# Performance work log

Measured on AMD Instinct MI355X. Metric: run time of the kernel, lower is better.

## Reference

```python
import jax, jax.numpy as jnp
import numpy as np

WD, WH, WW = 2, 7, 7          # window size (d, h, w)
N = WD * WH * WW              # 98 tokens per window
DIM = 768
NH = 24
HD = DIM // NH                # 32
SCALE = HD ** -0.5
NW = 64                       # windows per image
B = 4
B_ = B * NW                   # 256


def _relative_position_index():
    d, h, w = np.meshgrid(np.arange(WD), np.arange(WH), np.arange(WW), indexing='ij')
    coords = np.stack([d.ravel(), h.ravel(), w.ravel()])        # (3, N)
    rel = (coords[:, :, None] - coords[:, None, :]).transpose(1, 2, 0)  # (N, N, 3)
    rel = rel + np.array([WD - 1, WH - 1, WW - 1])
    rel = rel * np.array([(2 * WH - 1) * (2 * WW - 1), 2 * WW - 1, 1])
    return rel.sum(-1).astype(np.int32)                         # (N, N)


def setup_inputs() -> dict:
    key = jax.random.key(0)
    ks = jax.random.split(key, 5)
    table_rows = (2 * WD - 1) * (2 * WH - 1) * (2 * WW - 1)     # 507
    return {
        'x': jax.random.normal(ks[0], (B_, N, DIM), jnp.float32),
        'mask': jax.random.normal(ks[1], (NW, N, N), jnp.float32),
        'qkv_w': jax.random.normal(ks[2], (3 * DIM, DIM), jnp.float32) * 0.02,
        'qkv_b': jax.random.normal(ks[3], (3 * DIM,), jnp.float32) * 0.02,
        'rel_table': jax.random.normal(ks[4], (table_rows, NH), jnp.float32) * 0.02,
        'rel_index': jnp.asarray(_relative_position_index()),
    }


def reference(x, mask, qkv_w, qkv_b, rel_table, rel_index):
    Bs, n, c = x.shape
    # qkv linear; einops '(nH hD qkv)' => last dim factored as (nH, hD, 3)
    qkv = x @ qkv_w.T + qkv_b                                   # (Bs, N, 3C)
    qkv = qkv.reshape(Bs, n, NH, HD, 3)
    q, k, v = (jnp.moveaxis(qkv, -1, 0)                         # (3, Bs, N, nH, hD)
                  .transpose(0, 1, 3, 2, 4))                    # (3, Bs, nH, N, hD)
    attn = jnp.einsum('bhqd,bhkd->bhqk', q, k) * SCALE          # (Bs, nH, N, N)
    bias = rel_table[rel_index]                                 # (N, N, nH)
    attn = attn + bias.transpose(2, 0, 1)[None]                 # + (1, nH, N, N)
    # window mask add
    attn = attn.reshape(Bs // NW, NW, NH, n, n) + mask[None, :, None]
    attn = attn.reshape(Bs, NH, n, n)
    attn = jax.nn.softmax(attn, axis=-1)
    out = jnp.einsum('bhqk,bhkd->bhqd', attn, v)                # (Bs, nH, N, hD)
    return out.transpose(0, 2, 1, 3).reshape(Bs, n, c)          # (Bs, N, C)
```

## Files before the change

kernel.cpp:

```cpp
#include <hip/hip_runtime.h>
#include <hip/hip_bf16.h>
#include <stdint.h>


#define NTOK 98
#define MT 7
#define NPAD 112
#define DIMX 768
#define NHEAD 24
#define HDIM 32
#define NQKV 2304
#define BROWS 25088
#define SCALE 0.17677669529663689f
#define LOG2E 1.4426950408889634f
#define SCL2E (SCALE * LOG2E)
#define NN2 (NTOK * NTOK)
#define BMROW 112
#define BMSZ (BMROW * BMROW)
#define BMQ (BMSZ / 4)
#define PLANE ((size_t)BROWS * HDIM)

#define NB_X 18816
#define NB_W 1728
#define NB_BA 294
#define NB_B2 2352
#define GEMM_BLKS 3528

#if __has_builtin(__builtin_amdgcn_exp2f)
#define EXP2F(x) __builtin_amdgcn_exp2f(x)
#else
#define EXP2F(x) exp2f(x)
#endif

typedef __attribute__((ext_vector_type(8))) short short8;
typedef __attribute__((ext_vector_type(4))) short short4v;
typedef __attribute__((ext_vector_type(4))) float floatx4;

__device__ __forceinline__ short f2b(float f) {
    __hip_bfloat16 h = __float2bfloat16(f);
    return __builtin_bit_cast(short, h);
}
__device__ __forceinline__ float b2f(unsigned short s) {
    return __builtin_bit_cast(float, ((unsigned)s) << 16);
}

__device__ __forceinline__ void gload_lds16(const void* g, void* l) {
    __builtin_amdgcn_global_load_lds(
        (const __attribute__((address_space(1))) void*)g,
        (__attribute__((address_space(3))) void*)l, 16, 0, 0);
}

__device__ __forceinline__ void bm_body(int t,
                                        const float* __restrict__ rel_table,
                                        const int* __restrict__ rel_index,
                                        const float* __restrict__ mask,
                                        short* __restrict__ bm) {
    int wh = t / BMQ;
    int r4 = t % BMQ;
    int i = r4 / 28;
    int j0 = (r4 % 28) * 4;
    int h = wh % NHEAD, w = wh / NHEAD;
    short4v o;
    #pragma unroll
    for (int jj = 0; jj < 4; ++jj) {
        int j = j0 + jj;
        float val = -1e30f;
        if (i < NTOK && j < NTOK) {
            float bv = rel_table[(size_t)rel_index[i * NTOK + j] * NHEAD + h];
            float mv = mask[(size_t)w * NN2 + i * NTOK + j];
            val = (bv + mv) * LOG2E;
        }
        o[jj] = f2b(val);
    }
    *(short4v*)(bm + (size_t)wh * BMSZ + i * BMROW + j0) = o;
}

__global__ void prep_kernel(const float* __restrict__ x,
                            const float* __restrict__ w,
                            const float* __restrict__ rel_table,
                            const int* __restrict__ rel_index,
                            short* __restrict__ xb,
                            short* __restrict__ wb,
                            float* __restrict__ biasA) {
    int bid = blockIdx.x;
    if (bid < NB_X) {
        int i = bid * 256 + threadIdx.x;
        float4 f = ((const float4*)x)[i];
        short4v s = { f2b(f.x), f2b(f.y), f2b(f.z), f2b(f.w) };
        ((short4v*)xb)[i] = s;
    } else if (bid < NB_X + NB_W) {
        int i = (bid - NB_X) * 256 + threadIdx.x;
        int cp = i / 192, k4 = i % 192;
        int s = cp / DIMX, rem = cp % DIMX;
        int orig = (rem >> 5) * 96 + (rem & 31) * 3 + s;
        float sc = (s == 0) ? SCL2E : 1.0f;
        float4 f = ((const float4*)(w + (size_t)orig * DIMX))[k4];
        short4v o = { f2b(f.x * sc), f2b(f.y * sc), f2b(f.z * sc), f2b(f.w * sc) };
        ((short4v*)(wb + (size_t)cp * DIMX))[k4] = o;
    } else {
        int t = (bid - NB_X - NB_W) * 256 + threadIdx.x;
        int h = t / BMQ;
        int r4 = t % BMQ;
        int i = r4 / 28, j0 = (r4 % 28) * 4;
        float4 o;
        #pragma unroll
        for (int jj = 0; jj < 4; ++jj) {
            int j = j0 + jj;
            float val = -1e30f;
            if (i < NTOK && j < NTOK)
                val = rel_table[(size_t)rel_index[i * NTOK + j] * NHEAD + h] * LOG2E;
            o[jj] = val;
        }
        ((float4*)biasA)[t] = o;
    }
}

__global__ void bm_kernel(const float* __restrict__ rel_table,
                          const int* __restrict__ rel_index,
                          const float* __restrict__ mask,
                          short* __restrict__ bm) {
    int t = blockIdx.x * 256 + threadIdx.x;
    if (t >= 64 * NHEAD * BMQ) return;
    bm_body(t, rel_table, rel_index, mask, bm);
}

__global__ void bias_gather_kernel(const float* __restrict__ rel_table,
                                   const int* __restrict__ rel_index,
                                   float* __restrict__ bias_pre) {
    int t = blockIdx.x * 256 + threadIdx.x;
    if (t >= NHEAD * NN2) return;
    int h  = t / NN2;
    int ij = t % NN2;
    bias_pre[t] = rel_table[(size_t)rel_index[ij] * NHEAD + h];
}

__global__ void gemm_kernel(const short* __restrict__ xb,
                            const short* __restrict__ wb,
                            const float* __restrict__ qkv_b,
                            short* __restrict__ qkv,
                            const float* __restrict__ biasA,
                            const float* __restrict__ mask,
                            short* __restrict__ bm) {
    if (blockIdx.x >= GEMM_BLKS) {
        int base = (blockIdx.x - GEMM_BLKS) * 256 + threadIdx.x;
        #pragma unroll
        for (int it = 0; it < 8; ++it) {
            int t = base + it * (NB_B2 * 256);
            int wh = t / BMQ;
            int r4 = t % BMQ;
            int i = r4 / 28, j0 = (r4 % 28) * 4;
            int h = wh % NHEAD, w = wh / NHEAD;
            float4 ba = ((const float4*)biasA)[h * BMQ + r4];
            float m0 = 0.f, m1 = 0.f, m2 = 0.f, m3 = 0.f;
            if (i < NTOK && j0 < NTOK) {
                const float* mrow = mask + (size_t)w * NN2 + i * NTOK + j0;
                float2 a = *(const float2*)mrow;
                m0 = a.x; m1 = a.y;
                if (j0 < 96) {
                    float2 c = *(const float2*)(mrow + 2);
                    m2 = c.x; m3 = c.y;
                }
            }
            short4v o = { f2b(ba.x + m0 * LOG2E), f2b(ba.y + m1 * LOG2E),
                          f2b(ba.z + m2 * LOG2E), f2b(ba.w + m3 * LOG2E) };
            ((short4v*)bm)[t] = o;
        }
        return;
    }
    __shared__ short At[128 * 64];
    __shared__ short Bt[128 * 64];
    const int tid  = threadIdx.x;
    const int lane = tid & 63;
    const int wv   = tid >> 6;
    const int wr   = wv >> 1, wc = wv & 1;
    const int l15  = lane & 15;
    const int l4   = lane >> 4;

    int bid = blockIdx.x;
    int swz = (bid & 7) * 441 + (bid >> 3);
    const int mtile = swz / 18;
    const int ntile = swz % 18;

    const short* aB = xb + (size_t)(mtile * 128) * DIMX;
    const short* bB = wb + (size_t)(ntile * 128) * DIMX;
    const int lrow = lane >> 3;
    const int lcs  = (((lane & 7) ^ lrow) * 8);
    const int sa   = (l15 & 7) << 3;

    floatx4 acc[4][4];
    #pragma unroll
    for (int m = 0; m < 4; ++m)
        #pragma unroll
        for (int n = 0; n < 4; ++n) acc[m][n] = (floatx4){0.f, 0.f, 0.f, 0.f};

    for (int kb = 0; kb < 12; ++kb) {
        #pragma unroll
        for (int j = 0; j < 4; ++j) {
            int r = wv * 32 + j * 8;
            gload_lds16(aB + (size_t)(r + lrow) * DIMX + kb * 64 + lcs, &At[r * 64]);
            gload_lds16(bB + (size_t)(r + lrow) * DIMX + kb * 64 + lcs, &Bt[r * 64]);
        }
        __syncthreads();
        #pragma unroll
        for (int kh = 0; kh < 2; ++kh) {
            int k0 = kh * 32 + l4 * 8;
            int k0s = k0 ^ sa;
            short8 af[4], bfr[4];
            #pragma unroll
            for (int m = 0; m < 4; ++m)
                af[m] = *(const short8*)(&At[(wr * 64 + m * 16 + l15) * 64 + k0s]);
            #pragma unroll
            for (int n = 0; n < 4; ++n)
                bfr[n] = *(const short8*)(&Bt[(wc * 64 + n * 16 + l15) * 64 + k0s]);
            #pragma unroll
            for (int m = 0; m < 4; ++m)
                #pragma unroll
                for (int n = 0; n < 4; ++n)
                    acc[m][n] = __builtin_amdgcn_mfma_f32_16x16x32_bf16(
                        af[m], bfr[n], acc[m][n], 0, 0, 0);
        }
        __syncthreads();
    }

    #pragma unroll
    for (int n = 0; n < 4; ++n) {
        int col = ntile * 128 + wc * 64 + n * 16 + l15;
        int s = col / DIMX, rem = col % DIMX;
        int h2 = rem >> 5, d = rem & 31;
        int orig = h2 * 96 + d * 3 + s;
        float bias = qkv_b[orig] * ((s == 0) ? SCL2E : 1.0f);
        short* base = qkv + (size_t)(s * NHEAD + h2) * PLANE + d;
        #pragma unroll
        for (int m = 0; m < 4; ++m) {
            int row0 = mtile * 128 + wr * 64 + m * 16 + l4 * 4;
            #pragma unroll
            for (int r = 0; r < 4; ++r)
                base[(size_t)(row0 + r) * HDIM] = f2b(acc[m][n][r] + bias);
        }
    }
}

struct __align__(16) SMemC {
    short P[NPAD * 128];
    short q[NPAD * HDIM];
    short k[NPAD * HDIM];
    short vt[HDIM * 128];
};

__global__ __launch_bounds__(256, 3) void attn_kernel5(
    const short* __restrict__ qkv,
    const short* __restrict__ bm,
    float* __restrict__ out) {
    __shared__ SMemC sm;
    const int tid  = threadIdx.x;
    const int lane = tid & 63;
    const int wv   = tid >> 6;
    const int l15  = lane & 15;
    const int l4   = lane >> 4;
    int id = blockIdx.x;
    int nb = (id & 7) * 768 + (id >> 3);
    const int b = nb / NHEAD;
    const int h = nb % NHEAD;
    const short* qh = qkv + (size_t)h * PLANE            + (size_t)b * NTOK * HDIM;
    const short* kh = qkv + (size_t)(NHEAD + h) * PLANE  + (size_t)b * NTOK * HDIM;
    const short* vh = qkv + (size_t)(2 * NHEAD + h) * PLANE + (size_t)b * NTOK * HDIM;

    #pragma unroll
    for (int it = 0; it < 2; ++it) {
        int row0 = it * 64 + wv * 16;
        if (row0 < NTOK) {
            if (lane < (NTOK - row0) * 4) {
                gload_lds16(qh + row0 * HDIM + lane * 8, &sm.q[row0 * HDIM]);
                gload_lds16(kh + row0 * HDIM + lane * 8, &sm.k[row0 * HDIM]);
            }
        }
    }
    if (tid < 196) {
        int t = (tid >> 2) * 2, dh = tid & 3;
        const short* vp = vh + t * HDIM + dh * 8;
        short8 va = *(const short8*)vp;
        short8 vb = *(const short8*)(vp + HDIM);
        #pragma unroll
        for (int j = 0; j < 8; ++j) {
            int d = dh * 8 + j;
            int csw = t ^ ((d & 7) << 3);
            unsigned pk = ((unsigned)(unsigned short)vb[j] << 16) |
                          (unsigned)(unsigned short)va[j];
            *(unsigned*)(&sm.vt[d * 128 + csw]) = pk;
        }
    }
    if (tid < 112) {
        int a = tid / 56, r2 = (tid % 56) >> 2, seg = (tid & 3) * 8;
        short* dst = (a ? sm.k : sm.q) + (NTOK + r2) * HDIM + seg;
        *(uint4*)dst = (uint4){0u, 0u, 0u, 0u};
    }
    for (int t = tid; t < HDIM * 30; t += 256) {
        int d = t / 30, c = NTOK + t % 30;
        sm.vt[d * 128 + (c ^ ((d & 7) << 3))] = 0;
    }
    for (int t = tid; t < NPAD * 16; t += 256) {
        int r = t >> 4, c = 112 + (t & 15);
        sm.P[r * 128 + (c ^ ((r & 7) << 3))] = 0;
    }
    __syncthreads();

    int mt[2];
    mt[0] = wv;
    mt[1] = (wv + 4 < MT) ? (wv + 4) : wv;

    floatx4 sacc[2][7];
    #pragma unroll
    for (int i = 0; i < 2; ++i)
        #pragma unroll
        for (int j = 0; j < 7; ++j) sacc[i][j] = (floatx4){0.f, 0.f, 0.f, 0.f};
    {
        int k0 = l4 * 8;
        short8 bq[2];
        #pragma unroll
        for (int iq = 0; iq < 2; ++iq)
            bq[iq] = *(const short8*)(&sm.q[(mt[iq] * 16 + l15) * HDIM + k0]);
        __builtin_amdgcn_s_setprio(1);
        #pragma unroll
        for (int kt = 0; kt < 7; ++kt) {
            short8 ak = *(const short8*)(&sm.k[(kt * 16 + l15) * HDIM + k0]);
            #pragma unroll
            for (int iq = 0; iq < 2; ++iq)
                sacc[iq][kt] = __builtin_amdgcn_mfma_f32_16x16x32_bf16(
                    ak, bq[iq], sacc[iq][kt], 0, 0, 0);
        }
        __builtin_amdgcn_s_setprio(0);
    }

    const short* bmh = bm + ((size_t)(b & 63) * NHEAD + h) * BMSZ;
    const int swzp = (l15 & 7) << 3;

    #pragma unroll
    for (int iq = 0; iq < 2; ++iq) {
        int q = mt[iq] * 16 + l15;
        const short* bmq = bmh + q * BMROW + l4 * 4;
        float vv[7][4];
        #pragma unroll
        for (int kt = 0; kt < 7; ++kt) {
            short4v bm4 = *(const short4v*)(bmq + kt * 16);
            #pragma unroll
            for (int r = 0; r < 4; ++r)
                vv[kt][r] = sacc[iq][kt][r] + b2f((unsigned short)bm4[r]);
        }
        float mx = vv[0][0];
        #pragma unroll
        for (int kt = 0; kt < 7; ++kt)
            #pragma unroll
            for (int r = 0; r < 4; ++r) mx = fmaxf(mx, vv[kt][r]);
        mx = fmaxf(mx, __shfl_xor(mx, 16));
        mx = fmaxf(mx, __shfl_xor(mx, 32));
        float s = 0.f;
        #pragma unroll
        for (int kt = 0; kt < 7; ++kt)
            #pragma unroll
            for (int r = 0; r < 4; ++r) {
                float e = EXP2F(vv[kt][r] - mx);
                vv[kt][r] = e;
                s += e;
            }
        s += __shfl_xor(s, 16);
        s += __shfl_xor(s, 32);
        float inv = (q < NTOK) ? 1.f / s : 0.f;
        #pragma unroll
        for (int kt = 0; kt < 7; ++kt) {
            short4v pw = { f2b(vv[kt][0] * inv), f2b(vv[kt][1] * inv),
                           f2b(vv[kt][2] * inv), f2b(vv[kt][3] * inv) };
            *(short4v*)(&sm.P[q * 128 + ((kt * 16 + l4 * 4) ^ swzp)]) = pw;
        }
    }
    __syncthreads();

    floatx4 oacc[2][2];
    #pragma unroll
    for (int i = 0; i < 2; ++i)
        #pragma unroll
        for (int j = 0; j < 2; ++j) oacc[i][j] = (floatx4){0.f, 0.f, 0.f, 0.f};

    __builtin_amdgcn_s_setprio(1);
    #pragma unroll
    for (int kt = 0; kt < 4; ++kt) {
        int kk = (kt * 32 + l4 * 8) ^ swzp;
        short8 ap[2];
        #pragma unroll
        for (int im = 0; im < 2; ++im)
            ap[im] = *(const short8*)(&sm.P[(mt[im] * 16 + l15) * 128 + kk]);
        #pragma unroll
        for (int nt = 0; nt < 2; ++nt) {
            short8 bv = *(const short8*)(&sm.vt[(nt * 16 + l15) * 128 + kk]);
            #pragma unroll
            for (int im = 0; im < 2; ++im)
                oacc[im][nt] = __builtin_amdgcn_mfma_f32_16x16x32_bf16(
                    ap[im], bv, oacc[im][nt], 0, 0, 0);
        }
    }
    __builtin_amdgcn_s_setprio(0);

    float* ob = out + (size_t)b * NTOK * DIMX + h * HDIM;
    #pragma unroll
    for (int im = 0; im < 2; ++im)
        #pragma unroll
        for (int nt = 0; nt < 2; ++nt) {
            int dd = nt * 16 + l15;
            #pragma unroll
            for (int r = 0; r < 4; ++r) {
                int tok = mt[im] * 16 + l4 * 4 + r;
                if (tok < NTOK)
                    ob[(size_t)tok * DIMX + dd] = oacc[im][nt][r];
            }
        }
}

struct __align__(16) SMemF {
    union {
        struct {
            short xt[NPAD * 64];
            short wt[96 * 64];
        } p1;
        short P[NPAD * 128];
    } u;
    short q[NPAD * HDIM];
    short k[NPAD * HDIM];
    short vt[HDIM * 128];
};

__global__ __launch_bounds__(256, 3) void attn_fused(
    const float* __restrict__ x,
    const float* __restrict__ mask,
    const float* __restrict__ qkv_w,
    const float* __restrict__ qkv_b,
    const float* __restrict__ bias_pre,
    const float* __restrict__ rel_table,
    const int* __restrict__ rel_index,
    float* __restrict__ out) {
    __shared__ SMemF sm;
    const int tid  = threadIdx.x;
    const int lane = tid & 63;
    const int wv   = tid >> 6;
    const int l15  = lane & 15;
    const int l4   = lane >> 4;
    const int b = blockIdx.x / NHEAD;
    const int h = blockIdx.x % NHEAD;
    const float* xp = x + (size_t)b * NTOK * DIMX;
    const float* wp = qkv_w + (size_t)h * 96 * DIMX;
    int mt[2];
    mt[0] = wv;
    mt[1] = (wv + 4 < MT) ? (wv + 4) : wv;

    floatx4 acc[2][6];
    #pragma unroll
    for (int i = 0; i < 2; ++i)
        #pragma unroll
        for (int j = 0; j < 6; ++j) acc[i][j] = (floatx4){0.f, 0.f, 0.f, 0.f};

    for (int kb = 0; kb < 12; ++kb) {
        for (int t = tid; t < NTOK * 16; t += 256) {
            int row = t >> 4, c = t & 15;
            float4 f = *(const float4*)(xp + (size_t)row * DIMX + kb * 64 + c * 4);
            short4v s = { f2b(f.x), f2b(f.y), f2b(f.z), f2b(f.w) };
            *(short4v*)(&sm.u.p1.xt[row * 64 + c * 4]) = s;
        }
        for (int t = tid; t < 96 * 16; t += 256) {
            int row = t >> 4, c = t & 15;
            float4 f = *(const float4*)(wp + (size_t)row * DIMX + kb * 64 + c * 4);
            short4v s = { f2b(f.x), f2b(f.y), f2b(f.z), f2b(f.w) };
            *(short4v*)(&sm.u.p1.wt[row * 64 + c * 4]) = s;
        }
        if (tid < 14 * 8) {
            int row = 98 + (tid >> 3), c = tid & 7;
            uint4 z = {0u, 0u, 0u, 0u};
            *(uint4*)(&sm.u.p1.xt[row * 64 + c * 8]) = z;
        }
        __syncthreads();
        #pragma unroll
        for (int ks = 0; ks < 2; ++ks) {
            int k0 = ks * 32 + l4 * 8;
            short8 aM[2];
            #pragma unroll
            for (int im = 0; im < 2; ++im)
                aM[im] = *(const short8*)(&sm.u.p1.xt[(mt[im] * 16 + l15) * 64 + k0]);
            #pragma unroll
            for (int nt = 0; nt < 6; ++nt) {
                short8 bN = *(const short8*)(&sm.u.p1.wt[(nt * 16 + l15) * 64 + k0]);
                #pragma unroll
                for (int im = 0; im < 2; ++im)
                    acc[im][nt] = __builtin_amdgcn_mfma_f32_16x16x32_bf16(
                        aM[im], bN, acc[im][nt], 0, 0, 0);
            }
        }
        __syncthreads();
    }

    #pragma unroll
    for (int im = 0; im < 2; ++im)
        #pragma unroll
        for (int nt = 0; nt < 6; ++nt) {
            int col = nt * 16 + l15;
            int d = col / 3, s = col % 3;
            float bias = qkv_b[h * 96 + col];
            #pragma unroll
            for (int r = 0; r < 4; ++r) {
                int tok = mt[im] * 16 + l4 * 4 + r;
                short val = f2b(acc[im][nt][r] + bias);
                if (s == 0)      sm.q[tok * HDIM + d] = val;
                else if (s == 1) sm.k[tok * HDIM + d] = val;
                else             sm.vt[d * 128 + tok] = val;
            }
        }
    __syncthreads();
    for (int t = tid; t < HDIM * 30; t += 256) {
        int d = t / 30, c = 98 + t % 30;
        sm.vt[d * 128 + c] = 0;
    }
    for (int t = tid; t < NPAD * 16; t += 256) {
        int row = t >> 4, c = 112 + (t & 15);
        sm.u.P[row * 128 + c] = 0;
    }

    floatx4 sacc[2][7];
    #pragma unroll
    for (int i = 0; i < 2; ++i)
        #pragma unroll
        for (int j = 0; j < 7; ++j) sacc[i][j] = (floatx4){0.f, 0.f, 0.f, 0.f};
    {
        int k0 = l4 * 8;
        short8 aq[2];
        #pragma unroll
        for (int im = 0; im < 2; ++im)
            aq[im] = *(const short8*)(&sm.q[(mt[im] * 16 + l15) * HDIM + k0]);
        #pragma unroll
        for (int nt = 0; nt < 7; ++nt) {
            short8 bk = *(const short8*)(&sm.k[(nt * 16 + l15) * HDIM + k0]);
            #pragma unroll
            for (int im = 0; im < 2; ++im)
                sacc[im][nt] = __builtin_amdgcn_mfma_f32_16x16x32_bf16(
                    aq[im], bk, sacc[im][nt], 0, 0, 0);
        }
    }

    const float* biash = bias_pre ? (bias_pre + (size_t)h * NN2) : nullptr;
    const size_t moff = (size_t)(b & 63) * NN2;

    #pragma unroll
    for (int im = 0; im < 2; ++im)
        #pragma unroll
        for (int r = 0; r < 4; ++r) {
            int row = mt[im] * 16 + l4 * 4 + r;
            bool vrow = row < NTOK;
            float v[7];
            #pragma unroll
            for (int nt = 0; nt < 7; ++nt) {
                int j = nt * 16 + l15;
                bool vj = vrow && (j < NTOK);
                float bmv = 0.f;
                if (vj) {
                    float bias = biash ? biash[row * NTOK + j]
                        : rel_table[(size_t)rel_index[row * NTOK + j] * NHEAD + h];
                    bmv = bias + mask[moff + row * NTOK + j];
                }
                v[nt] = vj ? sacc[im][nt][r] * SCALE + bmv : -1e30f;
            }
            float mx = v[0];
            #pragma unroll
            for (int nt = 1; nt < 7; ++nt) mx = fmaxf(mx, v[nt]);
            #pragma unroll
            for (int off = 1; off < 16; off <<= 1) mx = fmaxf(mx, __shfl_xor(mx, off));
            float s = 0.f;
            #pragma unroll
            for (int nt = 0; nt < 7; ++nt) {
                float e = (v[nt] > -1e29f) ? __expf(v[nt] - mx) : 0.f;
                v[nt] = e;
                s += e;
            }
            #pragma unroll
            for (int off = 1; off < 16; off <<= 1) s += __shfl_xor(s, off);
            float inv = vrow ? 1.f / s : 0.f;
            #pragma unroll
            for (int nt = 0; nt < 7; ++nt)
                sm.u.P[row * 128 + nt * 16 + l15] = f2b(v[nt] * inv);
        }
    __syncthreads();

    floatx4 oacc[2][2];
    #pragma unroll
    for (int i = 0; i < 2; ++i)
        #pragma unroll
        for (int j = 0; j < 2; ++j) oacc[i][j] = (floatx4){0.f, 0.f, 0.f, 0.f};
    #pragma unroll
    for (int kt = 0; kt < 4; ++kt) {
        int kk = kt * 32 + l4 * 8;
        short8 ap[2];
        #pragma unroll
        for (int im = 0; im < 2; ++im)
            ap[im] = *(const short8*)(&sm.u.P[(mt[im] * 16 + l15) * 128 + kk]);
        #pragma unroll
        for (int nt = 0; nt < 2; ++nt) {
            short8 bv = *(const short8*)(&sm.vt[(nt * 16 + l15) * 128 + kk]);
            #pragma unroll
            for (int im = 0; im < 2; ++im)
                oacc[im][nt] = __builtin_amdgcn_mfma_f32_16x16x32_bf16(
                    ap[im], bv, oacc[im][nt], 0, 0, 0);
        }
    }
    float* ob = out + (size_t)b * NTOK * DIMX + h * HDIM;
    #pragma unroll
    for (int im = 0; im < 2; ++im)
        #pragma unroll
        for (int nt = 0; nt < 2; ++nt) {
            int dd = nt * 16 + l15;
            #pragma unroll
            for (int r = 0; r < 4; ++r) {
                int tok = mt[im] * 16 + l4 * 4 + r;
                if (tok < NTOK)
                    ob[(size_t)tok * DIMX + dd] = oacc[im][nt][r];
            }
        }
}

extern "C" void kernel_launch(void* const* d_in, const int* in_sizes, int n_in,
                              void* d_out, int out_size, void* d_ws, size_t ws_size,
                              hipStream_t stream) {
    const float* x = (const float*)d_in[0];
    const float* mask = (const float*)d_in[1];
    const float* qkv_w = (const float*)d_in[2];
    const float* qkv_b = (const float*)d_in[3];
    const float* rel_table = (const float*)d_in[4];
    const int* rel_index = (const int*)d_in[5];
    for (int i = 0; i < n_in; ++i) {
        switch (in_sizes[i]) {
            case 256 * NTOK * DIMX:  x         = (const float*)d_in[i]; break;
            case 64 * NN2:           mask      = (const float*)d_in[i]; break;
            case 3 * DIMX * DIMX:    qkv_w     = (const float*)d_in[i]; break;
            case 3 * DIMX:           qkv_b     = (const float*)d_in[i]; break;
            case 507 * NHEAD:        rel_table = (const float*)d_in[i]; break;
            case NN2:                rel_index = (const int*)d_in[i]; break;
            default: break;
        }
    }
    float* out = (float*)d_out;

    const size_t xb_bytes    = (size_t)BROWS * DIMX * 2;
    const size_t wb_bytes    = (size_t)NQKV * DIMX * 2;
    const size_t qkv_bytes   = (size_t)BROWS * NQKV * 2;
    const size_t bm_bytes    = (size_t)64 * NHEAD * BMSZ * 2;
    const size_t biasA_bytes = (size_t)NHEAD * BMSZ * 4;
    const size_t total       = xb_bytes + wb_bytes + qkv_bytes;

    if (ws_size >= total + bm_bytes + biasA_bytes) {
        short* xb    = (short*)d_ws;
        short* wb    = (short*)((char*)d_ws + xb_bytes);
        short* qkv   = (short*)((char*)d_ws + xb_bytes + wb_bytes);
        short* bmp   = (short*)((char*)d_ws + total);
        float* biasA = (float*)((char*)d_ws + total + bm_bytes);

        prep_kernel<<<NB_X + NB_W + NB_BA, 256, 0, stream>>>(
            x, qkv_w, rel_table, rel_index, xb, wb, biasA);
        gemm_kernel<<<GEMM_BLKS + NB_B2, 256, 0, stream>>>(
            xb, wb, qkv_b, qkv, biasA, mask, bmp);
        attn_kernel5<<<256 * NHEAD, 256, 0, stream>>>(qkv, bmp, out);
    } else if (ws_size >= total) {
        short* xb  = (short*)d_ws;
        short* wb  = (short*)((char*)d_ws + xb_bytes);
        short* qkv = (short*)((char*)d_ws + xb_bytes + wb_bytes);
        short* bmp = (short*)d_ws;

        prep_kernel<<<NB_X + NB_W, 256, 0, stream>>>(
            x, qkv_w, rel_table, rel_index, xb, wb, nullptr);
        gemm_kernel<<<GEMM_BLKS, 256, 0, stream>>>(
            xb, wb, qkv_b, qkv, nullptr, mask, nullptr);
        int nbm = 64 * NHEAD * BMQ;
        bm_kernel<<<(nbm + 255) / 256, 256, 0, stream>>>(
            rel_table, rel_index, mask, bmp);
        attn_kernel5<<<256 * NHEAD, 256, 0, stream>>>(qkv, bmp, out);
    } else {
        const size_t bias_bytes = (size_t)NHEAD * NN2 * sizeof(float);
        float* bias_pre = (ws_size >= bias_bytes) ? (float*)d_ws : nullptr;
        if (bias_pre) {
            int nb = NHEAD * NN2;
            bias_gather_kernel<<<(nb + 255) / 256, 256, 0, stream>>>(rel_table, rel_index, bias_pre);
        }
        attn_fused<<<256 * NHEAD, 256, 0, stream>>>(x, mask, qkv_w, qkv_b,
                                                    bias_pre, rel_table, rel_index, out);
    }
}
```

Measured before the change: 310.2 us.

## Fuse mask add into attention kernel and drop precomputed bias-mask tensor

The per-window, per-head bf16 bias+mask tensor that the GEMM kernel used to build is removed. The attention kernel now reads the fp32 per-head relative bias and the raw fp32 mask directly and adds them in registers. The block-to-window mapping is also changed so that blocks on the same XCD share windows and heads, which should let mask and bias reads hit in L2. This removes a large write and read of the intermediate, in exchange for more global loads per attention block and bounds-checked mask loads. In the fallback path, biasA now aliases the start of the workspace, which also holds xb.

```diff
diff --git a/kernel.cpp b/kernel.cpp
--- a/kernel.cpp
+++ b/kernel.cpp
@@ -23,7 +23,6 @@
 #define NB_X 18816
 #define NB_W 1728
 #define NB_BA 294
-#define NB_B2 2352
 #define GEMM_BLKS 3528
 
 #if __has_builtin(__builtin_amdgcn_exp2f)
@@ -40,9 +39,6 @@
     __hip_bfloat16 h = __float2bfloat16(f);
     return __builtin_bit_cast(short, h);
 }
-__device__ __forceinline__ float b2f(unsigned short s) {
-    return __builtin_bit_cast(float, ((unsigned)s) << 16);
-}
 
 __device__ __forceinline__ void gload_lds16(const void* g, void* l) {
     __builtin_amdgcn_global_load_lds(
@@ -50,29 +46,23 @@
         (__attribute__((address_space(3))) void*)l, 16, 0, 0);
 }
 
-__device__ __forceinline__ void bm_body(int t,
-                                        const float* __restrict__ rel_table,
-                                        const int* __restrict__ rel_index,
-                                        const float* __restrict__ mask,
-                                        short* __restrict__ bm) {
-    int wh = t / BMQ;
+__device__ __forceinline__ void biasA_body(int t,
+                                           const float* __restrict__ rel_table,
+                                           const int* __restrict__ rel_index,
+                                           float* __restrict__ biasA) {
+    int h = t / BMQ;
     int r4 = t % BMQ;
-    int i = r4 / 28;
-    int j0 = (r4 % 28) * 4;
-    int h = wh % NHEAD, w = wh / NHEAD;
-    short4v o;
+    int i = r4 / 28, j0 = (r4 % 28) * 4;
+    float4 o;
     #pragma unroll
     for (int jj = 0; jj < 4; ++jj) {
         int j = j0 + jj;
         float val = -1e30f;
-        if (i < NTOK && j < NTOK) {
-            float bv = rel_table[(size_t)rel_index[i * NTOK + j] * NHEAD + h];
-            float mv = mask[(size_t)w * NN2 + i * NTOK + j];
-            val = (bv + mv) * LOG2E;
-        }
-        o[jj] = f2b(val);
-    }
-    *(short4v*)(bm + (size_t)wh * BMSZ + i * BMROW + j0) = o;
+        if (i < NTOK && j < NTOK)
+            val = rel_table[(size_t)rel_index[i * NTOK + j] * NHEAD + h] * LOG2E;
+        o[jj] = val;
+    }
+    ((float4*)biasA)[t] = o;
 }
 
 __global__ void prep_kernel(const float* __restrict__ x,
@@ -99,29 +89,16 @@
         ((short4v*)(wb + (size_t)cp * DIMX))[k4] = o;
     } else {
         int t = (bid - NB_X - NB_W) * 256 + threadIdx.x;
-        int h = t / BMQ;
-        int r4 = t % BMQ;
-        int i = r4 / 28, j0 = (r4 % 28) * 4;
-        float4 o;
-        #pragma unroll
-        for (int jj = 0; jj < 4; ++jj) {
-            int j = j0 + jj;
-            float val = -1e30f;
-            if (i < NTOK && j < NTOK)
-                val = rel_table[(size_t)rel_index[i * NTOK + j] * NHEAD + h] * LOG2E;
-            o[jj] = val;
-        }
-        ((float4*)biasA)[t] = o;
-    }
-}
-
-__global__ void bm_kernel(const float* __restrict__ rel_table,
-                          const int* __restrict__ rel_index,
-                          const float* __restrict__ mask,
-                          short* __restrict__ bm) {
+        biasA_body(t, rel_table, rel_index, biasA);
+    }
+}
+
+__global__ void biasA_kernel(const float* __restrict__ rel_table,
+                             const int* __restrict__ rel_index,
+                             float* __restrict__ biasA) {
     int t = blockIdx.x * 256 + threadIdx.x;
-    if (t >= 64 * NHEAD * BMQ) return;
-    bm_body(t, rel_table, rel_index, mask, bm);
+    if (t >= NHEAD * BMQ) return;
+    biasA_body(t, rel_table, rel_index, biasA);
 }
 
 __global__ void bias_gather_kernel(const float* __restrict__ rel_table,
@@ -137,36 +114,7 @@
 __global__ void gemm_kernel(const short* __restrict__ xb,
                             const short* __restrict__ wb,
                             const float* __restrict__ qkv_b,
-                            short* __restrict__ qkv,
-                            const float* __restrict__ biasA,
-                            const float* __restrict__ mask,
-                            short* __restrict__ bm) {
-    if (blockIdx.x >= GEMM_BLKS) {
-        int base = (blockIdx.x - GEMM_BLKS) * 256 + threadIdx.x;
-        #pragma unroll
-        for (int it = 0; it < 8; ++it) {
-            int t = base + it * (NB_B2 * 256);
-            int wh = t / BMQ;
-            int r4 = t % BMQ;
-            int i = r4 / 28, j0 = (r4 % 28) * 4;
-            int h = wh % NHEAD, w = wh / NHEAD;
-            float4 ba = ((const float4*)biasA)[h * BMQ + r4];
-            float m0 = 0.f, m1 = 0.f, m2 = 0.f, m3 = 0.f;
-            if (i < NTOK && j0 < NTOK) {
-                const float* mrow = mask + (size_t)w * NN2 + i * NTOK + j0;
-                float2 a = *(const float2*)mrow;
-                m0 = a.x; m1 = a.y;
-                if (j0 < 96) {
-                    float2 c = *(const float2*)(mrow + 2);
-                    m2 = c.x; m3 = c.y;
-                }
-            }
-            short4v o = { f2b(ba.x + m0 * LOG2E), f2b(ba.y + m1 * LOG2E),
-                          f2b(ba.z + m2 * LOG2E), f2b(ba.w + m3 * LOG2E) };
-            ((short4v*)bm)[t] = o;
-        }
-        return;
-    }
+                            short* __restrict__ qkv) {
     __shared__ short At[128 * 64];
     __shared__ short Bt[128 * 64];
     const int tid  = threadIdx.x;
@@ -247,9 +195,10 @@
     short vt[HDIM * 128];
 };
 
-__global__ __launch_bounds__(256, 3) void attn_kernel5(
+__global__ __launch_bounds__(256, 3) void attn_kernel6(
     const short* __restrict__ qkv,
-    const short* __restrict__ bm,
+    const float* __restrict__ biasA,
+    const float* __restrict__ mask,
     float* __restrict__ out) {
     __shared__ SMemC sm;
     const int tid  = threadIdx.x;
@@ -258,9 +207,13 @@
     const int l15  = lane & 15;
     const int l4   = lane >> 4;
     int id = blockIdx.x;
-    int nb = (id & 7) * 768 + (id >> 3);
-    const int b = nb / NHEAD;
-    const int h = nb % NHEAD;
+    int xcd = id & 7, slot = id >> 3;
+    int w_local = slot / 96;
+    int rem = slot % 96;
+    int rep = rem / 24;
+    const int h = rem % 24;
+    int w = xcd * 8 + w_local;
+    const int b = rep * 64 + w;
     const short* qh = qkv + (size_t)h * PLANE            + (size_t)b * NTOK * HDIM;
     const short* kh = qkv + (size_t)(NHEAD + h) * PLANE  + (size_t)b * NTOK * HDIM;
     const short* vh = qkv + (size_t)(2 * NHEAD + h) * PLANE + (size_t)b * NTOK * HDIM;
@@ -331,20 +284,37 @@
         __builtin_amdgcn_s_setprio(0);
     }
 
-    const short* bmh = bm + ((size_t)(b & 63) * NHEAD + h) * BMSZ;
+    const float* bah = biasA + (size_t)h * BMSZ;
+    const float* mw  = mask + (size_t)(b & 63) * NN2;
     const int swzp = (l15 & 7) << 3;
 
     #pragma unroll
     for (int iq = 0; iq < 2; ++iq) {
         int q = mt[iq] * 16 + l15;
-        const short* bmq = bmh + q * BMROW + l4 * 4;
+        const float* bap = bah + q * BMROW + l4 * 4;
+        const float* mp  = mw  + q * NTOK  + l4 * 4;
+        bool qv = q < NTOK;
         float vv[7][4];
         #pragma unroll
         for (int kt = 0; kt < 7; ++kt) {
-            short4v bm4 = *(const short4v*)(bmq + kt * 16);
-            #pragma unroll
-            for (int r = 0; r < 4; ++r)
-                vv[kt][r] = sacc[iq][kt][r] + b2f((unsigned short)bm4[r]);
+            float4 ba = *(const float4*)(bap + kt * 16);
+            float m0 = 0.f, m1 = 0.f, m2 = 0.f, m3 = 0.f;
+            if (kt < 6) {
+                if (qv) {
+                    float2 a = *(const float2*)(mp + kt * 16);
+                    float2 c = *(const float2*)(mp + kt * 16 + 2);
+                    m0 = a.x; m1 = a.y; m2 = c.x; m3 = c.y;
+                }
+            } else {
+                if (qv && l4 == 0) {
+                    float2 a = *(const float2*)(mp + 96);
+                    m0 = a.x; m1 = a.y;
+                }
+            }
+            vv[kt][0] = sacc[iq][kt][0] + ba.x + m0 * LOG2E;
+            vv[kt][1] = sacc[iq][kt][1] + ba.y + m1 * LOG2E;
+            vv[kt][2] = sacc[iq][kt][2] + ba.z + m2 * LOG2E;
+            vv[kt][3] = sacc[iq][kt][3] + ba.w + m3 * LOG2E;
         }
         float mx = vv[0][0];
         #pragma unroll
@@ -364,7 +334,7 @@
             }
         s += __shfl_xor(s, 16);
         s += __shfl_xor(s, 32);
-        float inv = (q < NTOK) ? 1.f / s : 0.f;
+        float inv = qv ? 1.f / s : 0.f;
         #pragma unroll
         for (int kt = 0; kt < 7; ++kt) {
             short4v pw = { f2b(vv[kt][0] * inv), f2b(vv[kt][1] * inv),
@@ -645,36 +615,30 @@
     const size_t xb_bytes    = (size_t)BROWS * DIMX * 2;
     const size_t wb_bytes    = (size_t)NQKV * DIMX * 2;
     const size_t qkv_bytes   = (size_t)BROWS * NQKV * 2;
-    const size_t bm_bytes    = (size_t)64 * NHEAD * BMSZ * 2;
     const size_t biasA_bytes = (size_t)NHEAD * BMSZ * 4;
     const size_t total       = xb_bytes + wb_bytes + qkv_bytes;
 
-    if (ws_size >= total + bm_bytes + biasA_bytes) {
+    if (ws_size >= total + biasA_bytes) {
         short* xb    = (short*)d_ws;
         short* wb    = (short*)((char*)d_ws + xb_bytes);
         short* qkv   = (short*)((char*)d_ws + xb_bytes + wb_bytes);
-        short* bmp   = (short*)((char*)d_ws + total);
-        float* biasA = (float*)((char*)d_ws + total + bm_bytes);
+        float* biasA = (float*)((char*)d_ws + total);
 
         prep_kernel<<<NB_X + NB_W + NB_BA, 256, 0, stream>>>(
             x, qkv_w, rel_table, rel_index, xb, wb, biasA);
-        gemm_kernel<<<GEMM_BLKS + NB_B2, 256, 0, stream>>>(
-            xb, wb, qkv_b, qkv, biasA, mask, bmp);
-        attn_kernel5<<<256 * NHEAD, 256, 0, stream>>>(qkv, bmp, out);
+        gemm_kernel<<<GEMM_BLKS, 256, 0, stream>>>(xb, wb, qkv_b, qkv);
+        attn_kernel6<<<256 * NHEAD, 256, 0, stream>>>(qkv, biasA, mask, out);
     } else if (ws_size >= total) {
-        short* xb  = (short*)d_ws;
-        short* wb  = (short*)((char*)d_ws + xb_bytes);
-        short* qkv = (short*)((char*)d_ws + xb_bytes + wb_bytes);
-        short* bmp = (short*)d_ws;
+        short* xb    = (short*)d_ws;
+        short* wb    = (short*)((char*)d_ws + xb_bytes);
+        short* qkv   = (short*)((char*)d_ws + xb_bytes + wb_bytes);
+        float* biasA = (float*)d_ws;
 
         prep_kernel<<<NB_X + NB_W, 256, 0, stream>>>(
             x, qkv_w, rel_table, rel_index, xb, wb, nullptr);
-        gemm_kernel<<<GEMM_BLKS, 256, 0, stream>>>(
-            xb, wb, qkv_b, qkv, nullptr, mask, nullptr);
-        int nbm = 64 * NHEAD * BMQ;
-        bm_kernel<<<(nbm + 255) / 256, 256, 0, stream>>>(
-            rel_table, rel_index, mask, bmp);
-        attn_kernel5<<<256 * NHEAD, 256, 0, stream>>>(qkv, bmp, out);
+        gemm_kernel<<<GEMM_BLKS, 256, 0, stream>>>(xb, wb, qkv_b, qkv);
+        biasA_kernel<<<NB_BA, 256, 0, stream>>>(rel_table, rel_index, biasA);
+        attn_kernel6<<<256 * NHEAD, 256, 0, stream>>>(qkv, biasA, mask, out);
     } else {
         const size_t bias_bytes = (size_t)NHEAD * NN2 * sizeof(float);
         float* bias_pre = (ws_size >= bias_bytes) ? (float*)d_ws : nullptr;
```

Result: slower. 338.0 us (+9.0%).
